# Optimization experiments

Hardware: AMD Instinct MI355X
Metric: run time of the kernel (lower is better)

The kernel has to match this reference:

```python
import jax, jax.numpy as jnp
import numpy as np

B, T, S = 8, 8192, 128
VD, LD, E, H = 256, 768, 256, 8
HD = E // H
SCALE = HD ** -0.5
NEG = -9e15


def setup_inputs() -> dict:
    key = jax.random.key(0)
    ks = jax.random.split(key, 16)
    def xavier(k, shape):
        fan_in, fan_out = shape[1], shape[0]
        lim = np.sqrt(6.0 / (fan_in + fan_out))
        return jax.random.uniform(k, shape, jnp.float32, -lim, lim)
    return {
        "v": jax.random.normal(ks[0], (B, T, VD), jnp.float32),
        "l": jax.random.normal(ks[1], (B, S, LD), jnp.float32),
        "v_pos": jax.random.normal(ks[2], (B, T, VD), jnp.float32),
        "attention_mask_l": jnp.ones((B, S), jnp.int32),
        "attention_mask_v": jnp.ones((B, T), jnp.int32),
        "Wv": xavier(ks[3], (E, VD)),  "bv": jnp.zeros((E,), jnp.float32),
        "Wl": xavier(ks[4], (E, LD)),  "bl": jnp.zeros((E,), jnp.float32),
        "Wvv": xavier(ks[5], (E, VD)), "bvv": jnp.zeros((E,), jnp.float32),
        "Wvl": xavier(ks[6], (E, LD)), "bvl": jnp.zeros((E,), jnp.float32),
        "Wov": xavier(ks[7], (VD, E)), "bov": jnp.zeros((VD,), jnp.float32),
        "Wol": xavier(ks[8], (LD, E)), "bol": jnp.zeros((LD,), jnp.float32),
    }


def _heads(x):  # [B, N, E] -> [B, H, N, HD]
    Bn, N, _ = x.shape
    return x.reshape(Bn, N, H, HD).transpose(0, 2, 1, 3)


def reference(v, l, v_pos, attention_mask_l, attention_mask_v,
              Wv, bv, Wl, bl, Wvv, bvv, Wvl, bvl, Wov, bov, Wol, bol):
    # projections
    q = _heads(((v + v_pos) @ Wv.T + bv) * SCALE)   # [B,H,T,HD]
    k = _heads(l @ Wl.T + bl)                        # [B,H,S,HD]
    val_v = _heads(v @ Wvv.T + bvv)                  # [B,H,T,HD]
    val_l = _heads(l @ Wvl.T + bvl)                  # [B,H,S,HD]

    # shared score matrix
    attn = jnp.einsum("bhtd,bhsd->bhts", q, k)       # [B,H,T,S]

    # language -> vision direction (softmax over vision tokens T)
    attn_T = attn.transpose(0, 1, 3, 2)              # [B,H,S,T]
    attn_l = attn_T - jnp.max(attn_T, axis=-1, keepdims=True)
    mv = attention_mask_v.astype(jnp.float32)
    add_v = jnp.where(mv == 0, NEG, mv)[:, None, None, :]  # [B,1,1,T]
    attn_l = jax.nn.softmax(attn_l + add_v, axis=-1)

    # vision -> language direction (softmax over language tokens S)
    ml = attention_mask_l.astype(jnp.float32)
    add_l = jnp.where(ml == 0, NEG, ml)[:, None, None, :]  # [B,1,1,S]
    attn_v = jax.nn.softmax(attn + add_l, axis=-1)

    # dropout p=0.1 is identity in eval mode
    out_v = jnp.einsum("bhts,bhsd->bhtd", attn_v, val_l)  # [B,H,T,HD]
    out_l = jnp.einsum("bhst,bhtd->bhsd", attn_l, val_v)  # [B,H,S,HD]

    out_v = out_v.transpose(0, 2, 1, 3).reshape(B, T, E) @ Wov.T + bov
    out_l = out_l.transpose(0, 2, 1, 3).reshape(B, S, E) @ Wol.T + bol
    return out_v, out_l
```

## Files before the change

### kernel.cpp

```cpp
#include <hip/hip_runtime.h>

#define B_ 8
#define T_ 8192
#define S_ 128
#define VD_ 256
#define LD_ 768
#define E_ 256
#define H_ 8
#define HD_ 32
#define TC_ 8
#define SCALE_ 0.17677669529663687f
#define NEG_ -9.0e15f

typedef __bf16 bf16x8 __attribute__((ext_vector_type(8)));
typedef float f32x4 __attribute__((ext_vector_type(4)));
typedef unsigned int uint4v __attribute__((ext_vector_type(4)));

__device__ inline float bf2f(unsigned short u) {
    return __uint_as_float(((unsigned int)u) << 16);
}
__device__ inline unsigned short f2bf(float f) {
    unsigned int u = __float_as_uint(f);
    u = u + 0x7FFFu + ((u >> 16) & 1u);
    return (unsigned short)(u >> 16);
}
__device__ inline unsigned int pkbf(float lo, float hi) {
    unsigned short a = __builtin_bit_cast(unsigned short, (__bf16)lo);
    unsigned short b = __builtin_bit_cast(unsigned short, (__bf16)hi);
    return (unsigned int)a | ((unsigned int)b << 16);
}
__device__ inline bf16x8 lds8(const unsigned short* p) {
    uint4v v = *reinterpret_cast<const uint4v*>(p);
    return __builtin_bit_cast(bf16x8, v);
}

template<typename T>
__device__ inline uint4v load8_as_bf16(const T* p);

template<> __device__ inline uint4v load8_as_bf16<unsigned short>(const unsigned short* p) {
    return *reinterpret_cast<const uint4v*>(p);
}
template<> __device__ inline uint4v load8_as_bf16<float>(const float* p) {
    f32x4 f0 = reinterpret_cast<const f32x4*>(p)[0];
    f32x4 f1 = reinterpret_cast<const f32x4*>(p)[1];
    uint4v r;
    #pragma unroll
    for (int jj = 0; jj < 2; ++jj) {
        r[jj]     = (unsigned int)f2bf(f0[jj*2]) | ((unsigned int)f2bf(f0[jj*2+1]) << 16);
        r[jj + 2] = (unsigned int)f2bf(f1[jj*2]) | ((unsigned int)f2bf(f1[jj*2+1]) << 16);
    }
    return r;
}
__device__ inline uint4v load8_add_as_bf16(const float* p, const float* p2) {
    f32x4 a0 = reinterpret_cast<const f32x4*>(p)[0];
    f32x4 a1 = reinterpret_cast<const f32x4*>(p)[1];
    f32x4 b0 = reinterpret_cast<const f32x4*>(p2)[0];
    f32x4 b1 = reinterpret_cast<const f32x4*>(p2)[1];
    a0 += b0; a1 += b1;
    uint4v r;
    #pragma unroll
    for (int jj = 0; jj < 2; ++jj) {
        r[jj]     = (unsigned int)f2bf(a0[jj*2]) | ((unsigned int)f2bf(a0[jj*2+1]) << 16);
        r[jj + 2] = (unsigned int)f2bf(a1[jj*2]) | ((unsigned int)f2bf(a1[jj*2+1]) << 16);
    }
    return r;
}

template<typename TA, typename TW, typename TOUT, bool HAS_A2, bool SCALED>
__global__ __launch_bounds__(256) void gemm_bt(
    const TA* __restrict__ A, const TA* __restrict__ A2,
    const TW* __restrict__ W, const float* __restrict__ bias,
    TOUT* __restrict__ C, int M, int N, int K, float scale)
{
    __shared__ __align__(16) unsigned short As[64][72];
    __shared__ __align__(16) unsigned short Ws[64][72];
    const int tid  = threadIdx.x;
    const int lane = tid & 63;
    const int w    = tid >> 6;
    const int wm   = w >> 1, wn = w & 1;
    const int m0   = blockIdx.x * 64, n0 = blockIdx.y * 64;
    const int row  = tid >> 2, c0 = tid & 3;
    const int qd   = lane >> 4, lr = lane & 15;
    const f32x4 zero = {0.f, 0.f, 0.f, 0.f};
    f32x4 acc[2][2] = {{zero, zero}, {zero, zero}};

    for (int k0 = 0; k0 < K; k0 += 64) {
        #pragma unroll
        for (int cc = 0; cc < 2; ++cc) {
            int c = c0 + cc * 4;
            const TA* pa = A + (size_t)(m0 + row) * K + k0 + c * 8;
            uint4v va;
            if constexpr (HAS_A2) {
                const TA* pa2 = A2 + (size_t)(m0 + row) * K + k0 + c * 8;
                va = load8_add_as_bf16(pa, pa2);
            } else {
                va = load8_as_bf16<TA>(pa);
            }
            *reinterpret_cast<uint4v*>(&As[row][c * 8]) = va;
            const TW* pw = W + (size_t)(n0 + row) * K + k0 + c * 8;
            *reinterpret_cast<uint4v*>(&Ws[row][c * 8]) = load8_as_bf16<TW>(pw);
        }
        __syncthreads();
        #pragma unroll
        for (int ks = 0; ks < 2; ++ks) {
            bf16x8 af[2], bfr[2];
            #pragma unroll
            for (int i = 0; i < 2; ++i)
                af[i] = lds8(&As[wm * 32 + i * 16 + lr][ks * 32 + qd * 8]);
            #pragma unroll
            for (int i = 0; i < 2; ++i)
                bfr[i] = lds8(&Ws[wn * 32 + i * 16 + lr][ks * 32 + qd * 8]);
            #pragma unroll
            for (int i = 0; i < 2; ++i)
                #pragma unroll
                for (int j = 0; j < 2; ++j)
                    acc[i][j] = __builtin_amdgcn_mfma_f32_16x16x32_bf16(
                        af[i], bfr[j], acc[i][j], 0, 0, 0);
        }
        __syncthreads();
    }
    #pragma unroll
    for (int j = 0; j < 2; ++j) {
        int col = n0 + wn * 32 + j * 16 + lr;
        float bval = bias[col];
        #pragma unroll
        for (int i = 0; i < 2; ++i) {
            int r0 = m0 + wm * 32 + i * 16 + qd * 4;
            #pragma unroll
            for (int r = 0; r < 4; ++r) {
                float v = acc[i][j][r] + bval;
                if (SCALED) v *= scale;
                if constexpr (sizeof(TOUT) == 2)
                    C[(size_t)(r0 + r) * N + col] = (TOUT)f2bf(v);
                else
                    C[(size_t)(r0 + r) * N + col] = (TOUT)v;
            }
        }
    }
}

template<typename TA, typename TOUT, bool HAS_A2, bool SCALED>
__global__ __launch_bounds__(512) void gemm_ws(
    const TA* __restrict__ A, const float* __restrict__ A2,
    const float* __restrict__ Wf, const float* __restrict__ bias,
    TOUT* __restrict__ C, float scale)
{
    __shared__ __align__(16) unsigned short Ws[256 * 256];
    const int tid  = threadIdx.x;
    const int lane = tid & 63;
    const int w    = tid >> 6;
    const int quad = lane >> 4, lr = lane & 15;

    {
        const int row = tid >> 1;
        const int gb  = (tid & 1) * 16;
        #pragma unroll 8
        for (int i = 0; i < 16; ++i) {
            const int g  = gb + i;
            const int gs = g ^ (row & 7);
            uint4v val = load8_as_bf16<float>(Wf + (size_t)row * 256 + g * 8);
            *reinterpret_cast<uint4v*>(&Ws[row * 256 + gs * 8]) = val;
        }
    }

    const int r0 = blockIdx.x * 256 + w * 32;
    bf16x8 af[2][8];
    #pragma unroll
    for (int i = 0; i < 2; ++i) {
        const int row = r0 + i * 16 + lr;
        #pragma unroll
        for (int kq = 0; kq < 8; ++kq) {
            if constexpr (sizeof(TA) == 2) {
                af[i][kq] = lds8(reinterpret_cast<const unsigned short*>(A)
                                 + (size_t)row * 256 + quad * 8 + kq * 32);
            } else {
                const float* pa = reinterpret_cast<const float*>(A)
                                  + (size_t)row * 256 + quad * 8 + kq * 32;
                f32x4 a0 = reinterpret_cast<const f32x4*>(pa)[0];
                f32x4 a1 = reinterpret_cast<const f32x4*>(pa)[1];
                if constexpr (HAS_A2) {
                    const float* pp = A2 + (size_t)row * 256 + quad * 8 + kq * 32;
                    a0 += reinterpret_cast<const f32x4*>(pp)[0];
                    a1 += reinterpret_cast<const f32x4*>(pp)[1];
                }
                uint4v u;
                u[0] = pkbf(a0[0], a0[1]); u[1] = pkbf(a0[2], a0[3]);
                u[2] = pkbf(a1[0], a1[1]); u[3] = pkbf(a1[2], a1[3]);
                af[i][kq] = __builtin_bit_cast(bf16x8, u);
            }
        }
    }
    __syncthreads();

    const f32x4 zero = {0.f, 0.f, 0.f, 0.f};
    const int swz = lr & 7;
    for (int j = 0; j < 16; ++j) {
        const unsigned short* wbase = &Ws[(j * 16 + lr) * 256];
        f32x4 acc0 = zero, acc1 = zero;
        #pragma unroll
        for (int kq = 0; kq < 8; ++kq) {
            const int gs = (kq * 4 + quad) ^ swz;
            bf16x8 bw = lds8(wbase + gs * 8);
            acc0 = __builtin_amdgcn_mfma_f32_16x16x32_bf16(af[0][kq], bw, acc0, 0, 0, 0);
            acc1 = __builtin_amdgcn_mfma_f32_16x16x32_bf16(af[1][kq], bw, acc1, 0, 0, 0);
        }
        const int col = j * 16 + lr;
        const float bval = bias[col];
        #pragma unroll
        for (int r = 0; r < 4; ++r) {
            float v0 = acc0[r] + bval;
            float v1 = acc1[r] + bval;
            if constexpr (SCALED) { v0 *= scale; v1 *= scale; }
            if constexpr (sizeof(TOUT) == 2) {
                C[(size_t)(r0 + quad * 4 + r) * 256 + col]      = (TOUT)f2bf(v0);
                C[(size_t)(r0 + 16 + quad * 4 + r) * 256 + col] = (TOUT)f2bf(v1);
            } else {
                C[(size_t)(r0 + quad * 4 + r) * 256 + col]      = (TOUT)v0;
                C[(size_t)(r0 + 16 + quad * 4 + r) * 256 + col] = (TOUT)v1;
            }
        }
    }
}

__global__ __launch_bounds__(256) void attn_v_kernel(
    const unsigned short* __restrict__ q, const unsigned short* __restrict__ k,
    const unsigned short* __restrict__ vall, const int* __restrict__ mask_l,
    unsigned short* __restrict__ hv)
{
    __shared__ __align__(16) unsigned short Pl[64][136];
    __shared__ __align__(16) unsigned short Vt[32][136];
    const int tid  = threadIdx.x;
    const int lane = tid & 63;
    const int w    = tid >> 6;
    const int bh   = blockIdx.y, b = bh >> 3, h = bh & 7;
    const int t0   = blockIdx.x * 64;
    const int quad = lane >> 4, lr = lane & 15;
    const f32x4 zero = {0.f, 0.f, 0.f, 0.f};

    {
        int s = tid >> 1, dh = (tid & 1) * 16;
        const unsigned short* p = vall + (size_t)(b * S_ + s) * E_ + h * HD_ + dh;
        #pragma unroll
        for (int part = 0; part < 2; ++part) {
            uint4v v = reinterpret_cast<const uint4v*>(p)[part];
            #pragma unroll
            for (int jj = 0; jj < 4; ++jj) {
                unsigned int u = v[jj];
                int d = dh + part * 8 + jj * 2;
                Vt[d][s]     = (unsigned short)(u & 0xffffu);
                Vt[d + 1][s] = (unsigned short)(u >> 16);
            }
        }
    }

    bf16x8 afq = lds8(q + (size_t)(b * T_ + t0 + w * 16 + lr) * E_ + h * HD_ + quad * 8);
    f32x4 sc[8];
    #pragma unroll
    for (int n = 0; n < 8; ++n) {
        bf16x8 bk = lds8(k + (size_t)(b * S_ + n * 16 + lr) * E_ + h * HD_ + quad * 8);
        sc[n] = __builtin_amdgcn_mfma_f32_16x16x32_bf16(afq, bk, zero, 0, 0, 0);
    }
    #pragma unroll
    for (int n = 0; n < 8; ++n) {
        int s = n * 16 + lr;
        int mv = mask_l[b * S_ + s];
        float ad = (mv == 0) ? NEG_ : (float)mv;
        #pragma unroll
        for (int r = 0; r < 4; ++r) sc[n][r] += ad;
    }
    #pragma unroll
    for (int r = 0; r < 4; ++r) {
        float m = -3.0e38f;
        #pragma unroll
        for (int n = 0; n < 8; ++n) m = fmaxf(m, sc[n][r]);
        for (int off = 1; off < 16; off <<= 1) m = fmaxf(m, __shfl_xor(m, off));
        float sum = 0.f;
        #pragma unroll
        for (int n = 0; n < 8; ++n) { float e = __expf(sc[n][r] - m); sc[n][r] = e; sum += e; }
        for (int off = 1; off < 16; off <<= 1) sum += __shfl_xor(sum, off);
        float inv = 1.0f / sum;
        #pragma unroll
        for (int n = 0; n < 8; ++n) sc[n][r] *= inv;
    }
    #pragma unroll
    for (int n = 0; n < 8; ++n)
        #pragma unroll
        for (int r = 0; r < 4; ++r)
            Pl[w * 16 + quad * 4 + r][n * 16 + lr] = f2bf(sc[n][r]);
    __syncthreads();
    f32x4 av[2] = {zero, zero};
    #pragma unroll
    for (int ks = 0; ks < 4; ++ks) {
        bf16x8 ap = lds8(&Pl[w * 16 + lr][ks * 32 + quad * 8]);
        #pragma unroll
        for (int nn = 0; nn < 2; ++nn) {
            bf16x8 bv = lds8(&Vt[nn * 16 + lr][ks * 32 + quad * 8]);
            av[nn] = __builtin_amdgcn_mfma_f32_16x16x32_bf16(ap, bv, av[nn], 0, 0, 0);
        }
    }
    #pragma unroll
    for (int nn = 0; nn < 2; ++nn)
        #pragma unroll
        for (int r = 0; r < 4; ++r) {
            int t = t0 + w * 16 + quad * 4 + r;
            hv[(size_t)(b * T_ + t) * E_ + h * HD_ + nn * 16 + lr] = f2bf(av[nn][r]);
        }
}

__global__ __launch_bounds__(256) void attn_l_kernel(
    const unsigned short* __restrict__ q, const unsigned short* __restrict__ k,
    const unsigned short* __restrict__ valv, const int* __restrict__ mask_v,
    float* __restrict__ pM, float* __restrict__ pL, float* __restrict__ pA)
{
    __shared__ __align__(16) unsigned short Et[128][72];
    __shared__ __align__(16) unsigned short Vt[32][72];
    const int tid  = threadIdx.x;
    const int lane = tid & 63;
    const int w    = tid >> 6;
    const int bh   = blockIdx.y, b = bh >> 3, h = bh & 7;
    const int chunk = blockIdx.x;
    const int quad = lane >> 4, lr = lane & 15;
    const int sw0  = w * 32;
    const f32x4 zero = {0.f, 0.f, 0.f, 0.f};

    bf16x8 kf[2];
    #pragma unroll
    for (int mi = 0; mi < 2; ++mi)
        kf[mi] = lds8(k + (size_t)(b * S_ + sw0 + mi * 16 + lr) * E_ + h * HD_ + quad * 8);

    float mrun[2][4], lrun[2][4];
    #pragma unroll
    for (int mi = 0; mi < 2; ++mi)
        #pragma unroll
        for (int r = 0; r < 4; ++r) { mrun[mi][r] = -3.0e38f; lrun[mi][r] = 0.f; }
    f32x4 accl[2][2] = {{zero, zero}, {zero, zero}};

    const int titer = T_ / TC_ / 64;
    for (int it = 0; it < titer; ++it) {
        int t0 = chunk * (T_ / TC_) + it * 64;
        __syncthreads();
        {
            int t = tid >> 2, dq = tid & 3;
            const unsigned short* p = valv + (size_t)(b * T_ + t0 + t) * E_ + h * HD_ + dq * 8;
            uint4v v = *reinterpret_cast<const uint4v*>(p);
            #pragma unroll
            for (int jj = 0; jj < 4; ++jj) {
                unsigned int u = v[jj];
                Vt[dq * 8 + jj * 2][t]     = (unsigned short)(u & 0xffffu);
                Vt[dq * 8 + jj * 2 + 1][t] = (unsigned short)(u >> 16);
            }
        }
        f32x4 sc[2][4];
        #pragma unroll
        for (int n = 0; n < 4; ++n) {
            bf16x8 qf = lds8(q + (size_t)(b * T_ + t0 + n * 16 + lr) * E_ + h * HD_ + quad * 8);
            #pragma unroll
            for (int mi = 0; mi < 2; ++mi)
                sc[mi][n] = __builtin_amdgcn_mfma_f32_16x16x32_bf16(kf[mi], qf, zero, 0, 0, 0);
        }
        #pragma unroll
        for (int n = 0; n < 4; ++n) {
            int t = t0 + n * 16 + lr;
            int mv = mask_v[b * T_ + t];
            float ad = (mv == 0) ? NEG_ : (float)mv;
            #pragma unroll
            for (int mi = 0; mi < 2; ++mi)
                #pragma unroll
                for (int r = 0; r < 4; ++r) sc[mi][n][r] += ad;
        }
        #pragma unroll
        for (int mi = 0; mi < 2; ++mi)
            #pragma unroll
            for (int r = 0; r < 4; ++r) {
                float lm = -3.0e38f;
                #pragma unroll
                for (int n = 0; n < 4; ++n) lm = fmaxf(lm, sc[mi][n][r]);
                for (int off = 1; off < 16; off <<= 1) lm = fmaxf(lm, __shfl_xor(lm, off));
                float mnew = fmaxf(mrun[mi][r], lm);
                float alpha = __expf(mrun[mi][r] - mnew);
                float sum = 0.f;
                #pragma unroll
                for (int n = 0; n < 4; ++n) {
                    float e = __expf(sc[mi][n][r] - mnew); sc[mi][n][r] = e; sum += e;
                }
                for (int off = 1; off < 16; off <<= 1) sum += __shfl_xor(sum, off);
                lrun[mi][r] = lrun[mi][r] * alpha + sum;
                mrun[mi][r] = mnew;
                #pragma unroll
                for (int dn = 0; dn < 2; ++dn) accl[mi][dn][r] *= alpha;
            }
        #pragma unroll
        for (int mi = 0; mi < 2; ++mi)
            #pragma unroll
            for (int n = 0; n < 4; ++n)
                #pragma unroll
                for (int r = 0; r < 4; ++r)
                    Et[sw0 + mi * 16 + quad * 4 + r][n * 16 + lr] = f2bf(sc[mi][n][r]);
        __syncthreads();
        #pragma unroll
        for (int ks = 0; ks < 2; ++ks)
            #pragma unroll
            for (int mi = 0; mi < 2; ++mi) {
                bf16x8 ae = lds8(&Et[sw0 + mi * 16 + lr][ks * 32 + quad * 8]);
                #pragma unroll
                for (int dn = 0; dn < 2; ++dn) {
                    bf16x8 bv = lds8(&Vt[dn * 16 + lr][ks * 32 + quad * 8]);
                    accl[mi][dn] = __builtin_amdgcn_mfma_f32_16x16x32_bf16(ae, bv, accl[mi][dn], 0, 0, 0);
                }
            }
    }
    int pc = bh * TC_ + chunk;
    #pragma unroll
    for (int mi = 0; mi < 2; ++mi)
        #pragma unroll
        for (int r = 0; r < 4; ++r) {
            int s = sw0 + mi * 16 + quad * 4 + r;
            if (lr == 0) {
                pM[(size_t)pc * 128 + s] = mrun[mi][r];
                pL[(size_t)pc * 128 + s] = lrun[mi][r];
            }
            #pragma unroll
            for (int dn = 0; dn < 2; ++dn)
                pA[((size_t)pc * 128 + s) * 32 + dn * 16 + lr] = accl[mi][dn][r];
        }
}

__global__ __launch_bounds__(128) void combine_kernel(
    const float* __restrict__ pM, const float* __restrict__ pL,
    const float* __restrict__ pA, unsigned short* __restrict__ hl)
{
    int bh = blockIdx.x, b = bh >> 3, h = bh & 7;
    int s = threadIdx.x;
    float mc[TC_], wcf[TC_];
    float M = -3.0e38f;
    for (int c = 0; c < TC_; ++c) {
        mc[c] = pM[(size_t)(bh * TC_ + c) * 128 + s];
        M = fmaxf(M, mc[c]);
    }
    float L = 0.f;
    for (int c = 0; c < TC_; ++c) {
        wcf[c] = __expf(mc[c] - M);
        L += pL[(size_t)(bh * TC_ + c) * 128 + s] * wcf[c];
    }
    float inv = 1.0f / L;
    for (int d = 0; d < 32; ++d) {
        float o = 0.f;
        for (int c = 0; c < TC_; ++c)
            o += pA[((size_t)(bh * TC_ + c) * 128 + s) * 32 + d] * wcf[c];
        hl[(size_t)(b * S_ + s) * E_ + h * HD_ + d] = f2bf(o * inv);
    }
}

extern "C" void kernel_launch(void* const* d_in, const int* in_sizes, int n_in,
                              void* d_out, int out_size, void* d_ws, size_t ws_size,
                              hipStream_t stream)
{
    const float* v    = (const float*)d_in[0];
    const float* l    = (const float*)d_in[1];
    const float* vpos = (const float*)d_in[2];
    const int* mask_l = (const int*)d_in[3];
    const int* mask_v = (const int*)d_in[4];
    const float* Wv   = (const float*)d_in[5];
    const float* bv   = (const float*)d_in[6];
    const float* Wl   = (const float*)d_in[7];
    const float* bl   = (const float*)d_in[8];
    const float* Wvv  = (const float*)d_in[9];
    const float* bvv  = (const float*)d_in[10];
    const float* Wvl  = (const float*)d_in[11];
    const float* bvl  = (const float*)d_in[12];
    const float* Wov  = (const float*)d_in[13];
    const float* bov  = (const float*)d_in[14];
    const float* Wol  = (const float*)d_in[15];
    const float* bol  = (const float*)d_in[16];

    char* ws = (char*)d_ws;
    unsigned short* qbuf = (unsigned short*)(ws + 0);
    unsigned short* vbuf = (unsigned short*)(ws + 33554432);
    unsigned short* kbuf = (unsigned short*)(ws + 67108864);
    unsigned short* vall = (unsigned short*)(ws + 67633152);
    unsigned short* hl   = (unsigned short*)(ws + 68157440);
    float* pM            = (float*)(ws + 68681728);
    float* pL            = (float*)(ws + 68943872);
    float* pA            = (float*)(ws + 69206016);

    float* out_v = (float*)d_out;
    float* out_l = out_v + (size_t)B_ * T_ * VD_;

    gemm_ws<float, unsigned short, true, true>
        <<<dim3(B_*T_/256), 512, 0, stream>>>(v, vpos, Wv, bv, qbuf, SCALE_);
    gemm_ws<float, unsigned short, false, false>
        <<<dim3(B_*T_/256), 512, 0, stream>>>(v, nullptr, Wvv, bvv, vbuf, 1.f);

    gemm_bt<float, float, unsigned short, false, false>
        <<<dim3(B_*S_/64, E_/64), 256, 0, stream>>>(l, nullptr, Wl, bl, kbuf, B_*S_, E_, LD_, 1.f);
    gemm_bt<float, float, unsigned short, false, false>
        <<<dim3(B_*S_/64, E_/64), 256, 0, stream>>>(l, nullptr, Wvl, bvl, vall, B_*S_, E_, LD_, 1.f);

    attn_l_kernel<<<dim3(TC_, B_*H_), 256, 0, stream>>>(qbuf, kbuf, vbuf, mask_v, pM, pL, pA);
    combine_kernel<<<dim3(B_*H_), 128, 0, stream>>>(pM, pL, pA, hl);
    attn_v_kernel<<<dim3(T_/64, B_*H_), 256, 0, stream>>>(qbuf, kbuf, vall, mask_l, vbuf);

    gemm_ws<unsigned short, float, false, false>
        <<<dim3(B_*T_/256), 512, 0, stream>>>(vbuf, nullptr, Wov, bov, out_v, 1.f);
    gemm_bt<unsigned short, float, float, false, false>
        <<<dim3(B_*S_/64, LD_/64), 256, 0, stream>>>(hl, nullptr, Wol, bol, out_l, B_*S_, LD_, E_, 1.f);
}
```

Measured before the change: 445.2 us.

## Double attn_l block to 512 threads, one 16-row S tile per wave, 128-wide T steps

The language-direction attention kernel now runs 8 waves per block instead of 4. Each wave owns 16 language rows instead of 32 and processes 128 vision tokens per iteration instead of 64. This halves the number of loop iterations and barriers and puts more waves on the 512-block grid, which is small for the device. The cost is larger LDS tiles, more score registers per wave, and the Q-fragment and mask loads being repeated across twice as many waves.

Measured after the change: 448.1 us. About the same (+0.7%).

```diff
diff --git a/kernel.cpp b/kernel.cpp
--- a/kernel.cpp
+++ b/kernel.cpp
@@ -307,37 +307,32 @@
         }
 }
 
-__global__ __launch_bounds__(256) void attn_l_kernel(
+__global__ __launch_bounds__(512) void attn_l_kernel(
     const unsigned short* __restrict__ q, const unsigned short* __restrict__ k,
     const unsigned short* __restrict__ valv, const int* __restrict__ mask_v,
     float* __restrict__ pM, float* __restrict__ pL, float* __restrict__ pA)
 {
-    __shared__ __align__(16) unsigned short Et[128][72];
-    __shared__ __align__(16) unsigned short Vt[32][72];
+    __shared__ __align__(16) unsigned short Et[128][136];
+    __shared__ __align__(16) unsigned short Vt[32][136];
     const int tid  = threadIdx.x;
     const int lane = tid & 63;
     const int w    = tid >> 6;
     const int bh   = blockIdx.y, b = bh >> 3, h = bh & 7;
     const int chunk = blockIdx.x;
     const int quad = lane >> 4, lr = lane & 15;
-    const int sw0  = w * 32;
+    const int sw0  = w * 16;
     const f32x4 zero = {0.f, 0.f, 0.f, 0.f};
 
-    bf16x8 kf[2];
-    #pragma unroll
-    for (int mi = 0; mi < 2; ++mi)
-        kf[mi] = lds8(k + (size_t)(b * S_ + sw0 + mi * 16 + lr) * E_ + h * HD_ + quad * 8);
-
-    float mrun[2][4], lrun[2][4];
-    #pragma unroll
-    for (int mi = 0; mi < 2; ++mi)
-        #pragma unroll
-        for (int r = 0; r < 4; ++r) { mrun[mi][r] = -3.0e38f; lrun[mi][r] = 0.f; }
-    f32x4 accl[2][2] = {{zero, zero}, {zero, zero}};
-
-    const int titer = T_ / TC_ / 64;
+    bf16x8 kf = lds8(k + (size_t)(b * S_ + sw0 + lr) * E_ + h * HD_ + quad * 8);
+
+    float mrun[4], lrun[4];
+    #pragma unroll
+    for (int r = 0; r < 4; ++r) { mrun[r] = -3.0e38f; lrun[r] = 0.f; }
+    f32x4 accl[2] = {zero, zero};
+
+    const int titer = T_ / TC_ / 128;
     for (int it = 0; it < titer; ++it) {
-        int t0 = chunk * (T_ / TC_) + it * 64;
+        int t0 = chunk * (T_ / TC_) + it * 128;
         __syncthreads();
         {
             int t = tid >> 2, dq = tid & 3;
@@ -350,79 +345,67 @@
                 Vt[dq * 8 + jj * 2 + 1][t] = (unsigned short)(u >> 16);
             }
         }
-        f32x4 sc[2][4];
-        #pragma unroll
-        for (int n = 0; n < 4; ++n) {
+        f32x4 sc[8];
+        #pragma unroll
+        for (int n = 0; n < 8; ++n) {
             bf16x8 qf = lds8(q + (size_t)(b * T_ + t0 + n * 16 + lr) * E_ + h * HD_ + quad * 8);
-            #pragma unroll
-            for (int mi = 0; mi < 2; ++mi)
-                sc[mi][n] = __builtin_amdgcn_mfma_f32_16x16x32_bf16(kf[mi], qf, zero, 0, 0, 0);
-        }
-        #pragma unroll
-        for (int n = 0; n < 4; ++n) {
+            sc[n] = __builtin_amdgcn_mfma_f32_16x16x32_bf16(kf, qf, zero, 0, 0, 0);
+        }
+        #pragma unroll
+        for (int n = 0; n < 8; ++n) {
             int t = t0 + n * 16 + lr;
             int mv = mask_v[b * T_ + t];
             float ad = (mv == 0) ? NEG_ : (float)mv;
             #pragma unroll
-            for (int mi = 0; mi < 2; ++mi)
-                #pragma unroll
-                for (int r = 0; r < 4; ++r) sc[mi][n][r] += ad;
-        }
-        #pragma unroll
-        for (int mi = 0; mi < 2; ++mi)
-            #pragma unroll
-            for (int r = 0; r < 4; ++r) {
-                float lm = -3.0e38f;
-                #pragma unroll
-                for (int n = 0; n < 4; ++n) lm = fmaxf(lm, sc[mi][n][r]);
-                for (int off = 1; off < 16; off <<= 1) lm = fmaxf(lm, __shfl_xor(lm, off));
-                float mnew = fmaxf(mrun[mi][r], lm);
-                float alpha = __expf(mrun[mi][r] - mnew);
-                float sum = 0.f;
-                #pragma unroll
-                for (int n = 0; n < 4; ++n) {
-                    float e = __expf(sc[mi][n][r] - mnew); sc[mi][n][r] = e; sum += e;
-                }
-                for (int off = 1; off < 16; off <<= 1) sum += __shfl_xor(sum, off);
-                lrun[mi][r] = lrun[mi][r] * alpha + sum;
-                mrun[mi][r] = mnew;
-                #pragma unroll
-                for (int dn = 0; dn < 2; ++dn) accl[mi][dn][r] *= alpha;
-            }
-        #pragma unroll
-        for (int mi = 0; mi < 2; ++mi)
-            #pragma unroll
-            for (int n = 0; n < 4; ++n)
-                #pragma unroll
-                for (int r = 0; r < 4; ++r)
-                    Et[sw0 + mi * 16 + quad * 4 + r][n * 16 + lr] = f2bf(sc[mi][n][r]);
+            for (int r = 0; r < 4; ++r) sc[n][r] += ad;
+        }
+        #pragma unroll
+        for (int r = 0; r < 4; ++r) {
+            float lm = -3.0e38f;
+            #pragma unroll
+            for (int n = 0; n < 8; ++n) lm = fmaxf(lm, sc[n][r]);
+            for (int off = 1; off < 16; off <<= 1) lm = fmaxf(lm, __shfl_xor(lm, off));
+            float mnew = fmaxf(mrun[r], lm);
+            float alpha = __expf(mrun[r] - mnew);
+            float sum = 0.f;
+            #pragma unroll
+            for (int n = 0; n < 8; ++n) {
+                float e = __expf(sc[n][r] - mnew); sc[n][r] = e; sum += e;
+            }
+            for (int off = 1; off < 16; off <<= 1) sum += __shfl_xor(sum, off);
+            lrun[r] = lrun[r] * alpha + sum;
+            mrun[r] = mnew;
+            accl[0][r] *= alpha;
+            accl[1][r] *= alpha;
+        }
+        #pragma unroll
+        for (int n = 0; n < 8; ++n)
+            #pragma unroll
+            for (int r = 0; r < 4; ++r)
+                Et[sw0 + quad * 4 + r][n * 16 + lr] = f2bf(sc[n][r]);
         __syncthreads();
         #pragma unroll
-        for (int ks = 0; ks < 2; ++ks)
-            #pragma unroll
-            for (int mi = 0; mi < 2; ++mi) {
-                bf16x8 ae = lds8(&Et[sw0 + mi * 16 + lr][ks * 32 + quad * 8]);
-                #pragma unroll
-                for (int dn = 0; dn < 2; ++dn) {
-                    bf16x8 bv = lds8(&Vt[dn * 16 + lr][ks * 32 + quad * 8]);
-                    accl[mi][dn] = __builtin_amdgcn_mfma_f32_16x16x32_bf16(ae, bv, accl[mi][dn], 0, 0, 0);
-                }
-            }
+        for (int ks = 0; ks < 4; ++ks) {
+            bf16x8 ae = lds8(&Et[sw0 + lr][ks * 32 + quad * 8]);
+            #pragma unroll
+            for (int dn = 0; dn < 2; ++dn) {
+                bf16x8 bv = lds8(&Vt[dn * 16 + lr][ks * 32 + quad * 8]);
+                accl[dn] = __builtin_amdgcn_mfma_f32_16x16x32_bf16(ae, bv, accl[dn], 0, 0, 0);
+            }
+        }
     }
     int pc = bh * TC_ + chunk;
     #pragma unroll
-    for (int mi = 0; mi < 2; ++mi)
-        #pragma unroll
-        for (int r = 0; r < 4; ++r) {
-            int s = sw0 + mi * 16 + quad * 4 + r;
-            if (lr == 0) {
-                pM[(size_t)pc * 128 + s] = mrun[mi][r];
-                pL[(size_t)pc * 128 + s] = lrun[mi][r];
-            }
-            #pragma unroll
-            for (int dn = 0; dn < 2; ++dn)
-                pA[((size_t)pc * 128 + s) * 32 + dn * 16 + lr] = accl[mi][dn][r];
-        }
+    for (int r = 0; r < 4; ++r) {
+        int s = sw0 + quad * 4 + r;
+        if (lr == 0) {
+            pM[(size_t)pc * 128 + s] = mrun[r];
+            pL[(size_t)pc * 128 + s] = lrun[r];
+        }
+        #pragma unroll
+        for (int dn = 0; dn < 2; ++dn)
+            pA[((size_t)pc * 128 + s) * 32 + dn * 16 + lr] = accl[dn][r];
+    }
 }
 
 __global__ __launch_bounds__(128) void combine_kernel(
@@ -496,7 +479,7 @@
     gemm_bt<float, float, unsigned short, false, false>
         <<<dim3(B_*S_/64, E_/64), 256, 0, stream>>>(l, nullptr, Wvl, bvl, vall, B_*S_, E_, LD_, 1.f);
 
-    attn_l_kernel<<<dim3(TC_, B_*H_), 256, 0, stream>>>(qbuf, kbuf, vbuf, mask_v, pM, pL, pA);
+    attn_l_kernel<<<dim3(TC_, B_*H_), 512, 0, stream>>>(qbuf, kbuf, vbuf, mask_v, pM, pL, pA);
     combine_kernel<<<dim3(B_*H_), 128, 0, stream>>>(pM, pL, pA, hl);
     attn_v_kernel<<<dim3(T_/64, B_*H_), 256, 0, stream>>>(qbuf, kbuf, vall, mask_l, vbuf);
 
```
